# Performance work log

Hardware: AMD Instinct MI355X
Metric: run time of the kernel (lower is better)

## Reference

```python
import jax, jax.numpy as jnp
import numpy as np

QB = 64  # quantize_size from the source


def _blockwise_quant(y):
    """y: (N, R, C) softmax output. Quantize in 64x64 tiles to int8.
    Returns (q_int8 [N*g1*g2, QB*QB], s, z) matching the torch code."""
    N, R, C = y.shape
    g1, g2 = R // QB, C // QB
    # (N, g1, QB, g2, QB) -> (N, g1, g2, QB, QB) -> (N*g1*g2, QB*QB)
    b = y.reshape(N, g1, QB, g2, QB).transpose(0, 1, 3, 2, 4).reshape(-1, QB * QB)
    mx = jnp.max(b, axis=-1, keepdims=True)
    mn = jnp.min(b, axis=-1, keepdims=True)
    s = (mx - mn) / 255.0
    z = -mn / (s + 1e-10) - 128.0
    q = jnp.round(jnp.clip(b / (s + 1e-10) + z, -128.0, 127.0)).astype(jnp.int8)
    return q, s, z


def reference(x):
    # Forward: plain softmax over dim=-1; the int8 blockwise quantization is the
    # activation saved for backward (returned here so the workload isn't DCE'd).
    out = jax.nn.softmax(x, axis=-1)
    y = out.reshape(-1, x.shape[-2], x.shape[-1])
    q, s, z = _blockwise_quant(y)
    return out, q, s, z


def setup_inputs():
    key = jax.random.key(0)
    x = jax.random.normal(key, (2, 16, 2048, 2048), dtype=jnp.float32)
    return {"x": x}
```

## Files before the change

kernel.cpp:

```cpp
#include <hip/hip_runtime.h>
#include <math.h>


static constexpr int  COLS      = 2048;
static constexpr long long OUT_ELEMS = 134217728LL;
static constexpr int  NROWS     = 65536;
static constexpr int  NBLK      = 32768;

__global__ __launch_bounds__(256) void rowstats_kernel(
    const float* __restrict__ x, float* __restrict__ stats)
{
    const int lane = threadIdx.x & 63;
    const int wave = threadIdx.x >> 6;
    const long long row = (long long)blockIdx.x * 4 + wave;
    const float* rp = x + row * COLS;

    float4 v[8];
#pragma unroll
    for (int c = 0; c < 8; ++c)
        v[c] = *reinterpret_cast<const float4*>(rp + c * 256 + lane * 4);

    float m = -INFINITY;
#pragma unroll
    for (int c = 0; c < 8; ++c)
        m = fmaxf(m, fmaxf(fmaxf(v[c].x, v[c].y), fmaxf(v[c].z, v[c].w)));
#pragma unroll
    for (int off = 32; off >= 1; off >>= 1)
        m = fmaxf(m, __shfl_xor(m, off, 64));

    float s = 0.0f;
#pragma unroll
    for (int c = 0; c < 8; ++c)
        s += expf(v[c].x - m) + expf(v[c].y - m) +
             expf(v[c].z - m) + expf(v[c].w - m);
#pragma unroll
    for (int off = 32; off >= 1; off >>= 1)
        s += __shfl_xor(s, off, 64);

    if (lane == 0) {
        stats[row * 2 + 0] = m;
        stats[row * 2 + 1] = 1.0f / s;
    }
}

__global__ __launch_bounds__(256) void tile_kernel(
    const float* __restrict__ x, const float* __restrict__ stats,
    float* __restrict__ out, float* __restrict__ qout,
    float* __restrict__ sout, float* __restrict__ zout)
{
    const int b = blockIdx.x;
    const int n = b >> 10;
    const int i = (b >> 5) & 31;
    const int j = b & 31;
    const int t = threadIdx.x;
    const int col4 = (t & 15) * 4;
    const int r0 = t >> 4;

    const long long xbase = (long long)n * (COLS * (long long)COLS)
                          + (long long)(i * 64) * COLS + j * 64;
    const int growbase = (n << 11) + i * 64;

    float4 p[4];
    float mn = INFINITY, mx = -INFINITY;
#pragma unroll
    for (int k = 0; k < 4; ++k) {
        const int r = r0 + k * 16;
        const float2 st = *reinterpret_cast<const float2*>(
            stats + (long long)(growbase + r) * 2);
        const float4 v = *reinterpret_cast<const float4*>(
            x + xbase + (long long)r * COLS + col4);
        float4 pv;
        pv.x = expf(v.x - st.x) * st.y;
        pv.y = expf(v.y - st.x) * st.y;
        pv.z = expf(v.z - st.x) * st.y;
        pv.w = expf(v.w - st.x) * st.y;
        p[k] = pv;
        mn = fminf(mn, fminf(fminf(pv.x, pv.y), fminf(pv.z, pv.w)));
        mx = fmaxf(mx, fmaxf(fmaxf(pv.x, pv.y), fmaxf(pv.z, pv.w)));
    }
#pragma unroll
    for (int off = 32; off >= 1; off >>= 1) {
        mn = fminf(mn, __shfl_xor(mn, off, 64));
        mx = fmaxf(mx, __shfl_xor(mx, off, 64));
    }

    __shared__ float smn[4], smx[4], sbc[2];
    const int wave = t >> 6;
    if ((t & 63) == 0) { smn[wave] = mn; smx[wave] = mx; }
    __syncthreads();
    if (t == 0) {
        const float bmn = fminf(fminf(smn[0], smn[1]), fminf(smn[2], smn[3]));
        const float bmx = fmaxf(fmaxf(smx[0], smx[1]), fmaxf(smx[2], smx[3]));
        const float sc = (bmx - bmn) / 255.0f;
        const float d  = sc + 1e-10f;
        const float zz = -bmn / d - 128.0f;
        sout[b] = sc;
        zout[b] = zz;
        sbc[0] = zz;
        sbc[1] = 1.0f / d;
    }
    __syncthreads();
    const float z = sbc[0], rcp = sbc[1];

    float* __restrict__ qb = qout + (long long)b * 4096;
#pragma unroll
    for (int k = 0; k < 4; ++k) {
        const int r = r0 + k * 16;
        const float4 pv = p[k];
        *reinterpret_cast<float4*>(out + xbase + (long long)r * COLS + col4) = pv;
        float4 qv;
        qv.x = roundf(fminf(fmaxf(pv.x * rcp + z, -128.0f), 127.0f));
        qv.y = roundf(fminf(fmaxf(pv.y * rcp + z, -128.0f), 127.0f));
        qv.z = roundf(fminf(fmaxf(pv.z * rcp + z, -128.0f), 127.0f));
        qv.w = roundf(fminf(fmaxf(pv.w * rcp + z, -128.0f), 127.0f));
        *reinterpret_cast<float4*>(qb + r * 64 + col4) = qv;
    }
}

extern "C" void kernel_launch(void* const* d_in, const int* in_sizes, int n_in,
                              void* d_out, int out_size, void* d_ws, size_t ws_size,
                              hipStream_t stream) {
    const float* x = (const float*)d_in[0];
    float* out  = (float*)d_out;
    float* qout = out + OUT_ELEMS;
    float* sout = qout + OUT_ELEMS;
    float* zout = sout + NBLK;
    float* stats = (float*)d_ws;

    rowstats_kernel<<<NROWS / 4, 256, 0, stream>>>(x, stats);
    tile_kernel<<<NBLK, 256, 0, stream>>>(x, stats, out, qout, sout, zout);
}
```

Measured before the change: 421.4 us.

## Process four quant tiles per block with full-row reads and nontemporal stores

The tile kernel is replaced by a panel kernel. Each block now covers a 64x256 panel, four 64x64 quant tiles, so every wave reads a contiguous 1 KB row segment instead of 16 short 256-byte pieces. Per-tile min/max is reduced over 16-lane groups and in shared memory, with four threads computing the scale and zero point. Output and quantized stores become nontemporal to avoid polluting the cache. Each thread now holds 16 float4 values, which raises register pressure and cuts the block count to 8192.

```diff
diff --git a/kernel.cpp b/kernel.cpp
--- a/kernel.cpp
+++ b/kernel.cpp
@@ -6,6 +6,8 @@
 static constexpr long long OUT_ELEMS = 134217728LL;
 static constexpr int  NROWS     = 65536;
 static constexpr int  NBLK      = 32768;
+
+using v4f = __attribute__((ext_vector_type(4))) float;
 
 __global__ __launch_bounds__(256) void rowstats_kernel(
     const float* __restrict__ x, float* __restrict__ stats)
@@ -43,32 +45,32 @@
     }
 }
 
-__global__ __launch_bounds__(256) void tile_kernel(
+__global__ __launch_bounds__(256) void panel_kernel(
     const float* __restrict__ x, const float* __restrict__ stats,
     float* __restrict__ out, float* __restrict__ qout,
     float* __restrict__ sout, float* __restrict__ zout)
 {
-    const int b = blockIdx.x;
-    const int n = b >> 10;
-    const int i = (b >> 5) & 31;
-    const int j = b & 31;
-    const int t = threadIdx.x;
-    const int col4 = (t & 15) * 4;
-    const int r0 = t >> 4;
+    const int b  = blockIdx.x;
+    const int n  = b >> 8;
+    const int i  = (b >> 3) & 31;
+    const int jg = b & 7;
+    const int t  = threadIdx.x;
+    const int w  = t >> 6;
+    const int l  = t & 63;
 
     const long long xbase = (long long)n * (COLS * (long long)COLS)
-                          + (long long)(i * 64) * COLS + j * 64;
+                          + (long long)(i * 64) * COLS + jg * 256;
     const int growbase = (n << 11) + i * 64;
 
-    float4 p[4];
+    float4 p[16];
     float mn = INFINITY, mx = -INFINITY;
 #pragma unroll
-    for (int k = 0; k < 4; ++k) {
-        const int r = r0 + k * 16;
+    for (int k = 0; k < 16; ++k) {
+        const int r = (k << 2) + w;
         const float2 st = *reinterpret_cast<const float2*>(
             stats + (long long)(growbase + r) * 2);
         const float4 v = *reinterpret_cast<const float4*>(
-            x + xbase + (long long)r * COLS + col4);
+            x + xbase + (long long)r * COLS + l * 4);
         float4 pv;
         pv.x = expf(v.x - st.x) * st.y;
         pv.y = expf(v.y - st.x) * st.y;
@@ -79,41 +81,48 @@
         mx = fmaxf(mx, fmaxf(fmaxf(pv.x, pv.y), fmaxf(pv.z, pv.w)));
     }
 #pragma unroll
-    for (int off = 32; off >= 1; off >>= 1) {
+    for (int off = 8; off >= 1; off >>= 1) {
         mn = fminf(mn, __shfl_xor(mn, off, 64));
         mx = fmaxf(mx, __shfl_xor(mx, off, 64));
     }
 
-    __shared__ float smn[4], smx[4], sbc[2];
-    const int wave = t >> 6;
-    if ((t & 63) == 0) { smn[wave] = mn; smx[wave] = mx; }
+    __shared__ float  smn[4][4], smx[4][4];
+    __shared__ float2 sbc[4];
+    if ((l & 15) == 0) { smn[w][l >> 4] = mn; smx[w][l >> 4] = mx; }
     __syncthreads();
-    if (t == 0) {
-        const float bmn = fminf(fminf(smn[0], smn[1]), fminf(smn[2], smn[3]));
-        const float bmx = fmaxf(fmaxf(smx[0], smx[1]), fmaxf(smx[2], smx[3]));
+    if (t < 4) {
+        const float bmn = fminf(fminf(smn[0][t], smn[1][t]),
+                                fminf(smn[2][t], smn[3][t]));
+        const float bmx = fmaxf(fmaxf(smx[0][t], smx[1][t]),
+                                fmaxf(smx[2][t], smx[3][t]));
         const float sc = (bmx - bmn) / 255.0f;
         const float d  = sc + 1e-10f;
         const float zz = -bmn / d - 128.0f;
-        sout[b] = sc;
-        zout[b] = zz;
-        sbc[0] = zz;
-        sbc[1] = 1.0f / d;
+        const int b4 = (n << 10) + (i << 5) + (jg << 2) + t;
+        sout[b4] = sc;
+        zout[b4] = zz;
+        sbc[t] = make_float2(zz, 1.0f / d);
     }
     __syncthreads();
-    const float z = sbc[0], rcp = sbc[1];
 
-    float* __restrict__ qb = qout + (long long)b * 4096;
+    const int   tl  = l >> 4;
+    const float2 bc = sbc[tl];
+    float* __restrict__ qb = qout
+        + (long long)((n << 10) + (i << 5) + (jg << 2)) * 4096
+        + tl * 4096 + (l & 15) * 4;
+
 #pragma unroll
-    for (int k = 0; k < 4; ++k) {
-        const int r = r0 + k * 16;
+    for (int k = 0; k < 16; ++k) {
+        const int r = (k << 2) + w;
         const float4 pv = p[k];
-        *reinterpret_cast<float4*>(out + xbase + (long long)r * COLS + col4) = pv;
+        __builtin_nontemporal_store(*(const v4f*)&pv,
+            (v4f*)(out + xbase + (long long)r * COLS + l * 4));
         float4 qv;
-        qv.x = roundf(fminf(fmaxf(pv.x * rcp + z, -128.0f), 127.0f));
-        qv.y = roundf(fminf(fmaxf(pv.y * rcp + z, -128.0f), 127.0f));
-        qv.z = roundf(fminf(fmaxf(pv.z * rcp + z, -128.0f), 127.0f));
-        qv.w = roundf(fminf(fmaxf(pv.w * rcp + z, -128.0f), 127.0f));
-        *reinterpret_cast<float4*>(qb + r * 64 + col4) = qv;
+        qv.x = roundf(fminf(fmaxf(pv.x * bc.y + bc.x, -128.0f), 127.0f));
+        qv.y = roundf(fminf(fmaxf(pv.y * bc.y + bc.x, -128.0f), 127.0f));
+        qv.z = roundf(fminf(fmaxf(pv.z * bc.y + bc.x, -128.0f), 127.0f));
+        qv.w = roundf(fminf(fmaxf(pv.w * bc.y + bc.x, -128.0f), 127.0f));
+        __builtin_nontemporal_store(*(const v4f*)&qv, (v4f*)(qb + r * 64));
     }
 }
 
@@ -128,5 +137,5 @@
     float* stats = (float*)d_ws;
 
     rowstats_kernel<<<NROWS / 4, 256, 0, stream>>>(x, stats);
-    tile_kernel<<<NBLK, 256, 0, stream>>>(x, stats, out, qout, sout, zout);
+    panel_kernel<<<8192, 256, 0, stream>>>(x, stats, out, qout, sout, zout);
 }
```

Measured after the change: 405.1 us, median of 2. 1.04x faster.
